# Optimization experiments

Hardware: AMD Instinct MI355X
Metric: run time of the kernel (lower is better)

The kernel has to match this reference:

```python
import jax, jax.numpy as jnp
import numpy as np

S = 1        # support_num
K = 20       # neighbor_num for conv stages
EPS_BN = 1e-5

def _normalize(x, axis):
    n = jnp.linalg.norm(x, axis=axis, keepdims=True)
    return x / jnp.maximum(n, 1e-12)

def _knn(verts, k):
    # verts: (b, v, 3) -> (b, v, k) nearest-neighbor indices excluding self
    sq = jnp.sum(verts * verts, axis=-1)                                   # (b, v)
    d = sq[:, :, None] + sq[:, None, :] - 2.0 * jnp.einsum('bic,bjc->bij', verts, verts)
    _, idx = jax.lax.top_k(-d, k + 1)                                      # smallest distances
    return idx[:, :, 1:]

def _gather(t, idx):
    # t: (b, v, c), idx: (b, v, n) -> (b, v, n, c)
    return jax.vmap(lambda tb, ib: tb[ib])(t, idx)

def _theta(nidx, verts, directions, out_c):
    # relu(cos angle) between normalized neighbor directions and support directions
    ndir = _normalize(_gather(verts, nidx) - verts[:, :, None, :], -1)     # (b, v, n, 3)
    sdir = _normalize(directions, 0)                                       # (3, S*out_c)
    th = jax.nn.relu(jnp.einsum('bvnc,ck->bvnk', ndir, sdir))
    b, v, n, _ = th.shape
    return th.reshape(b, v, n, S, out_c)

def _conv_surface(nidx, verts, directions, kernel_num):
    th = _theta(nidx, verts, directions, kernel_num)                       # (b,v,n,S,k)
    return th.max(axis=2).sum(axis=2)                                      # (b, v, k)

def _conv_layer(nidx, verts, fm, w, bias, directions, out_c):
    th = _theta(nidx, verts, directions, out_c)                            # (b,v,n,S,o)
    fout = fm @ w + bias                                                   # (b,v,(S+1)*o)
    center = fout[..., :out_c]
    support = _gather(fout[..., out_c:], nidx)                             # (b,v,n,S*o)
    b, v, n, _ = support.shape
    act = (th * support.reshape(b, v, n, S, out_c)).max(axis=2).sum(axis=2)
    return center + act

def _bn(x):
    # BatchNorm1d(affine=False) training-mode: per-channel over (batch, vertices)
    m = jnp.mean(x, axis=(0, 1))
    v = jnp.var(x, axis=(0, 1))
    return (x - m) * jax.lax.rsqrt(v + EPS_BN)

def _pool(verts, fm, rate, nk):
    nidx = _knn(verts, nk)
    pooled = _gather(fm, nidx).max(axis=2)
    pn = verts.shape[1] // rate
    # deterministic subsample (original uses randperm; fixed choice for a stable baseline)
    return verts[:, :pn], pooled[:, :pn]

def _forward(vertices, c0_dir, c1_w, c1_b, c1_dir, d1_w, c2_w, c2_b, c2_dir, d2_w,
             c3_w, c3_b, c3_dir, d3_w, c4_w, c4_b, c4_dir, d4_w,
             cls_w1, cls_b1, cls_g, cls_beta, cls_w2, cls_b2):
    verts = jnp.transpose(vertices, (0, 2, 1))                             # (b, N, 3)
    nidx = _knn(verts, K)
    fm0 = jax.nn.relu(_conv_surface(nidx, verts, c0_dir, 32))
    res1 = fm0 @ d1_w.T
    fm1 = jax.nn.relu(_bn(_conv_layer(nidx, verts, fm0, c1_w, c1_b, c1_dir, 64))) + res1
    verts, fm1 = _pool(verts, fm1, 4, 4)
    nidx = _knn(verts, K)
    res2 = fm1 @ d2_w.T
    fm2 = jax.nn.relu(_bn(_conv_layer(nidx, verts, fm1, c2_w, c2_b, c2_dir, 128))) + res2
    res3 = fm2 @ d3_w.T
    fm3 = jax.nn.relu(_bn(_conv_layer(nidx, verts, fm2, c3_w, c3_b, c3_dir, 256))) + res3
    verts, fm3 = _pool(verts, fm3, 4, 4)
    nidx = _knn(verts, K)
    res4 = fm3 @ d4_w.T
    fm4 = jax.nn.relu(_bn(_conv_layer(nidx, verts, fm3, c4_w, c4_b, c4_dir, 1024))) + res4
    g = fm4.max(axis=1)                                                    # (b, 1024)
    h = g @ cls_w1.T + cls_b1
    m = jnp.mean(h, axis=0); var = jnp.var(h, axis=0)                      # BN(256), dropout=eval identity
    h = (h - m) * jax.lax.rsqrt(var + EPS_BN) * cls_g + cls_beta
    h = jax.nn.relu(h)
    return h @ cls_w2.T + cls_b2                                           # (b, 40)

def setup_inputs() -> dict:
    key = jax.random.key(0)
    ks = jax.random.split(key, 24)
    def u(k, shape, s=0.05):
        return jax.random.uniform(k, shape, jnp.float32, -s, s)
    return {
        'vertices': jax.random.normal(ks[0], (32, 3, 1024), jnp.float32),
        'c0_dir': u(ks[1], (3, S * 32)),
        'c1_w': u(ks[2], (32, (S + 1) * 64)),  'c1_b': u(ks[3], ((S + 1) * 64,)),  'c1_dir': u(ks[4], (3, S * 64)),
        'd1_w': u(ks[5], (64, 32)),
        'c2_w': u(ks[6], (64, (S + 1) * 128)), 'c2_b': u(ks[7], ((S + 1) * 128,)), 'c2_dir': u(ks[8], (3, S * 128)),
        'd2_w': u(ks[9], (128, 64)),
        'c3_w': u(ks[10], (128, (S + 1) * 256)), 'c3_b': u(ks[11], ((S + 1) * 256,)), 'c3_dir': u(ks[12], (3, S * 256)),
        'd3_w': u(ks[13], (256, 128)),
        'c4_w': u(ks[14], (256, (S + 1) * 1024)), 'c4_b': u(ks[15], ((S + 1) * 1024,)), 'c4_dir': u(ks[16], (3, S * 1024)),
        'd4_w': u(ks[17], (1024, 256)),
        'cls_w1': u(ks[18], (256, 1024)), 'cls_b1': u(ks[19], (256,)),
        'cls_g': jnp.ones((256,), jnp.float32), 'cls_beta': jnp.zeros((256,), jnp.float32),
        'cls_w2': u(ks[20], (40, 256)), 'cls_b2': u(ks[21], (40,)),
    }

def reference(vertices, c0_dir, c1_w, c1_b, c1_dir, d1_w, c2_w, c2_b, c2_dir, d2_w,
              c3_w, c3_b, c3_dir, d3_w, c4_w, c4_b, c4_dir, d4_w,
              cls_w1, cls_b1, cls_g, cls_beta, cls_w2, cls_b2):
    return _forward(vertices, c0_dir, c1_w, c1_b, c1_dir, d1_w, c2_w, c2_b, c2_dir, d2_w,
                    c3_w, c3_b, c3_dir, d3_w, c4_w, c4_b, c4_dir, d4_w,
                    cls_w1, cls_b1, cls_g, cls_beta, cls_w2, cls_b2)
```

## Files before the change

kernel.cpp:

```cpp
#include <hip/hip_runtime.h>

#define TPB 256
#define KNN_TPB 512
static inline int nblk(long n) { return (int)((n + TPB - 1) / TPB); }

#define FINF 3.402823466e38f

template <int NS, bool WDIR, bool CSURF, int K2>
__device__ __forceinline__ void knn_body(int bx, int b, const float* __restrict__ vin,
                                         int* __restrict__ knn, float* __restrict__ ndir,
                                         int V_out, const float* __restrict__ c0dir,
                                         float* __restrict__ fm0, int V2, int* __restrict__ knn4,
                                         float4* pts, int (*sidx)[20], float (*sdir)[20][3],
                                         unsigned (*cdist)[256], unsigned short (*cidx)[256]) {
    constexpr int K = 20;
    constexpr int VF = NS * 64;
    const float* vb = vin + (size_t)b * 3072;
    for (int j = threadIdx.x; j < VF; j += blockDim.x) {
        float x = vb[j], y = vb[1024 + j], z = vb[2048 + j];
        pts[j] = make_float4(x, y, z, x * x + y * y + z * z);
    }
    __syncthreads();
    int lane = threadIdx.x & 63;
    int w = threadIdx.x >> 6;
    int i = bx * 8 + w;
    if (i >= V_out) return;
    float4 pi = pts[i];
    unsigned ud[NS];
    unsigned lmin = 0xFFFFFFFFu;
#pragma unroll
    for (int s = 0; s < NS; ++s) {
        int j = s * 64 + lane;
        float4 pj = pts[j];
        float dist = pi.w + pj.w - 2.f * (pi.x * pj.x + pi.y * pj.y + pi.z * pj.z);
        dist = fmaxf(dist, 0.f);
        unsigned v = (j == i) ? 0xFFFFFFFFu : __float_as_uint(dist);
        ud[s] = v;
        lmin = v < lmin ? v : lmin;
    }
    unsigned pmin = lmin;
    {
        unsigned o = (unsigned)__shfl_xor((int)pmin, 1, 64);
        pmin = o < pmin ? o : pmin;
    }
    unsigned gmin = lmin, M = pmin;
#pragma unroll
    for (int off = 32; off > 1; off >>= 1) {
        unsigned on = (unsigned)__shfl_xor((int)gmin, off, 64);
        gmin = on < gmin ? on : gmin;
        unsigned om = (unsigned)__shfl_xor((int)M, off, 64);
        M = om > M ? om : M;
    }
    {
        unsigned on = (unsigned)__shfl_xor((int)gmin, 1, 64);
        gmin = on < gmin ? on : gmin;
    }
    int* orow = knn + ((size_t)(b * V_out + i)) * K;
    unsigned long long lmask = (1ull << lane) - 1ull;
    bool done = false;
    if constexpr (NS >= 8) {
        int cnt = 0;
#pragma unroll
        for (int s = 0; s < NS; ++s) {
            unsigned long long mm = __ballot(ud[s] <= M);
            if (ud[s] <= M) {
                int p = cnt + __popcll(mm & lmask);
                if (p < 256) { cdist[w][p] = ud[s]; cidx[w][p] = (unsigned short)(s * 64 + lane); }
            }
            cnt += __popcll(mm);
        }
        if (cnt <= 256) {
            unsigned cd[4];
#pragma unroll
            for (int r = 0; r < 4; ++r) {
                int p = lane + r * 64;
                cd[r] = p < cnt ? cdist[w][p] : 0xFFFFFFFFu;
            }
            unsigned lo = gmin, hi = M + 1u;
            while (hi - lo > 1u) {
                unsigned mid = lo + ((hi - lo) >> 1);
                int c = 0;
#pragma unroll
                for (int r = 0; r < 4; ++r)
                    c += __popcll(__ballot(cd[r] < mid));
                if (c >= K) hi = mid; else lo = mid;
            }
            unsigned T = lo;
            int base = 0;
#pragma unroll
            for (int r = 0; r < 4; ++r) {
                unsigned long long mm = __ballot(cd[r] < T);
                if (cd[r] < T) {
                    int p = base + __popcll(mm & lmask);
                    int j = cidx[w][lane + r * 64];
                    sidx[w][p] = j; orow[p] = j;
                }
                base += __popcll(mm);
            }
            int need = K - base, run = 0;
#pragma unroll
            for (int r = 0; r < 4; ++r) {
                unsigned long long mm = __ballot(cd[r] == T);
                int rr = run + __popcll(mm & lmask);
                if (cd[r] == T && rr < need) {
                    int j = cidx[w][lane + r * 64];
                    sidx[w][base + rr] = j; orow[base + rr] = j;
                }
                run += __popcll(mm);
            }
            done = true;
        }
    }
    if (!done) {
        unsigned lo = gmin, hi = M + 1u;
        while (hi - lo > 1u) {
            unsigned mid = lo + ((hi - lo) >> 1);
            int cnt = 0;
#pragma unroll
            for (int s = 0; s < NS; ++s)
                cnt += __popcll(__ballot(ud[s] < mid));
            if (cnt >= K) hi = mid; else lo = mid;
        }
        unsigned T = lo;
        int base = 0;
#pragma unroll
        for (int s = 0; s < NS; ++s) {
            unsigned long long m = __ballot(ud[s] < T);
            if (ud[s] < T) {
                int p = base + __popcll(m & lmask);
                sidx[w][p] = s * 64 + lane;
                orow[p] = s * 64 + lane;
            }
            base += __popcll(m);
        }
        int need = K - base, run = 0;
#pragma unroll
        for (int s = 0; s < NS; ++s) {
            unsigned long long m = __ballot(ud[s] == T);
            int r = run + __popcll(m & lmask);
            if (ud[s] == T && r < need) {
                sidx[w][base + r] = s * 64 + lane;
                orow[base + r] = s * 64 + lane;
            }
            run += __popcll(m);
        }
    }
    if (WDIR) {
        if (lane < K) {
            int j = sidx[w][lane];
            float4 pj = pts[j];
            float dx = pj.x - pi.x, dy = pj.y - pi.y, dz = pj.z - pi.z;
            float inv = 1.f / fmaxf(sqrtf(dx * dx + dy * dy + dz * dz), 1e-12f);
            float* o = ndir + ((size_t)(b * V_out + i) * K + lane) * 3;
            float nx = dx * inv, ny = dy * inv, nz = dz * inv;
            o[0] = nx; o[1] = ny; o[2] = nz;
            if (CSURF) { sdir[w][lane][0] = nx; sdir[w][lane][1] = ny; sdir[w][lane][2] = nz; }
        }
        if (CSURF && lane < 32) {
            int c = lane;
            float d0 = c0dir[c], d1 = c0dir[32 + c], d2 = c0dir[64 + c];
            float inv = 1.f / fmaxf(sqrtf(d0 * d0 + d1 * d1 + d2 * d2), 1e-12f);
            d0 *= inv; d1 *= inv; d2 *= inv;
            float m = 0.f;
            for (int n = 0; n < K; ++n) {
                float th = sdir[w][n][0] * d0 + sdir[w][n][1] * d1 + sdir[w][n][2] * d2;
                m = fmaxf(m, th);
            }
            fm0[(size_t)(b * V_out + i) * 32 + c] = m;
        }
    }
    if (K2 > 0 && i < V2) {
        float dsel = FINF;
        int jsel = 0x7FFFFFFF;
        if (lane < K) {
            jsel = sidx[w][lane];
            float4 pj = pts[jsel];
            dsel = fmaxf(pi.w + pj.w - 2.f * (pi.x * pj.x + pi.y * pj.y + pi.z * pj.z), 0.f);
        }
        int rank = 0;
        for (int m = 0; m < K; ++m) {
            float dm = __shfl(dsel, m, 64);
            int jm = __shfl(jsel, m, 64);
            rank += (dm < dsel || (dm == dsel && jm < jsel)) ? 1 : 0;
        }
        if (lane < K && rank < K2) knn4[((size_t)(b * V2 + i)) * K2 + rank] = jsel;
    }
}

__global__ __launch_bounds__(KNN_TPB, 1) void prep_kernel(const float* __restrict__ vin, const float* __restrict__ c0dir,
                                                          int* __restrict__ knn1, float* __restrict__ ndir1,
                                                          float* __restrict__ fm0, int* __restrict__ knn4_1,
                                                          int* __restrict__ knn2, float* __restrict__ ndir2,
                                                          int* __restrict__ knn4_2,
                                                          int* __restrict__ knn3, float* __restrict__ ndir3,
                                                          const float* __restrict__ d1, const float* __restrict__ d2,
                                                          const float* __restrict__ d3, const float* __restrict__ d4,
                                                          float* __restrict__ o1, float* __restrict__ o2,
                                                          float* __restrict__ o3, float* __restrict__ o4,
                                                          float* __restrict__ pz) {
    __shared__ float4 pts[1024];
    __shared__ int sidx[8][20];
    __shared__ float sdir[8][20][3];
    __shared__ unsigned cdist[8][256];
    __shared__ unsigned short cidx[8][256];
    int bx = blockIdx.x, b = blockIdx.y;
    if (bx < 128) {
        knn_body<16, true, true, 4>(bx, b, vin, knn1, ndir1, 1024, c0dir, fm0, 256, knn4_1,
                                    pts, sidx, sdir, cdist, cidx);
        return;
    }
    if (bx < 160) {
        knn_body<4, true, false, 4>(bx - 128, b, vin, knn2, ndir2, 256, nullptr, nullptr, 64, knn4_2,
                                    pts, sidx, sdir, cdist, cidx);
        return;
    }
    if (bx < 168) {
        knn_body<1, true, false, 0>(bx - 160, b, vin, knn3, ndir3, 64, nullptr, nullptr, 0, nullptr,
                                    pts, sidx, sdir, cdist, cidx);
        return;
    }
    if (b != 0) return;
    if (bx < 764) {
        int t = (bx - 168) * KNN_TPB + threadIdx.x;
        if (t < 2048) { int r = t / 32, c = t % 32; o1[c * 64 + r] = d1[t]; return; }
        int t2 = t - 2048;
        if (t2 < 8192) { int r = t2 / 64, c = t2 % 64; o2[c * 128 + r] = d2[t2]; return; }
        int t3 = t2 - 8192;
        if (t3 < 32768) { int r = t3 / 128, c = t3 % 128; o3[c * 256 + r] = d3[t3]; return; }
        int t4 = t3 - 32768;
        if (t4 < 262144) { int r = t4 / 256, c = t4 % 256; o4[c * 1024 + r] = d4[t4]; }
        return;
    }
    int t5 = (bx - 764) * KNN_TPB + threadIdx.x;
    if (t5 < 57344) pz[t5] = 0.f;
}

template <int MODE>
__global__ __launch_bounds__(TPB) void gemm64_kernel(const float* __restrict__ A, const float* __restrict__ W,
                                                     const float* __restrict__ bias,
                                                     const float* __restrict__ conv, const float* __restrict__ partial,
                                                     float* __restrict__ out, int M, int N, int K, int nsplit) {
    __shared__ float As[64][36];
    __shared__ float Bs[32][68];
    __shared__ float smean[64], sinv[64];
    int t = threadIdx.x;
    int tx = t & 15, ty = t >> 4;
    int colbase = blockIdx.x * 64, rowbase = blockIdx.y * 64;
    int r0 = ty * 4, c0 = tx * 4;
    if constexpr (MODE >= 1) {
        __shared__ double sred[2][4][64];
        int cc = t & 63, g = t >> 6;
        double s = 0.0, ss = 0.0;
        for (int sp = g; sp < nsplit; sp += 4) {
            s += partial[(size_t)sp * 2 * N + colbase + cc];
            ss += partial[(size_t)sp * 2 * N + N + colbase + cc];
        }
        sred[0][g][cc] = s; sred[1][g][cc] = ss;
        __syncthreads();
        if (t < 64) {
            double S = sred[0][0][t] + sred[0][1][t] + sred[0][2][t] + sred[0][3][t];
            double SS = sred[1][0][t] + sred[1][1][t] + sred[1][2][t] + sred[1][3][t];
            double mean = S / M;
            double var = SS / M - mean * mean;
            if (var < 0) var = 0;
            smean[t] = (float)mean;
            sinv[t] = rsqrtf((float)var + 1e-5f);
        }
        __syncthreads();
    }
    float4 acc0, acc1, acc2, acc3;
    if (MODE == 0) {
        float4 bv = *(const float4*)(bias + colbase + c0);
        acc0 = bv; acc1 = bv; acc2 = bv; acc3 = bv;
    } else {
        acc0 = make_float4(0.f, 0.f, 0.f, 0.f); acc1 = acc0; acc2 = acc0; acc3 = acc0;
    }
    for (int kt = 0; kt < K; kt += 32) {
#pragma unroll
        for (int l = 0; l < 2; ++l) {
            int lin = t + l * 256;
            int ar = lin >> 3, ak = (lin & 7) << 2;
            *(float4*)&As[ar][ak] = *(const float4*)(A + (size_t)(rowbase + ar) * K + kt + ak);
            int br = lin >> 4, bn = (lin & 15) << 2;
            *(float4*)&Bs[br][bn] = *(const float4*)(W + (size_t)(kt + br) * N + colbase + bn);
        }
        __syncthreads();
#pragma unroll 4
        for (int k = 0; k < 32; ++k) {
            float4 bv = *(const float4*)&Bs[k][c0];
            float a0 = As[r0][k], a1 = As[r0 + 1][k], a2 = As[r0 + 2][k], a3 = As[r0 + 3][k];
            acc0.x += a0 * bv.x; acc0.y += a0 * bv.y; acc0.z += a0 * bv.z; acc0.w += a0 * bv.w;
            acc1.x += a1 * bv.x; acc1.y += a1 * bv.y; acc1.z += a1 * bv.z; acc1.w += a1 * bv.w;
            acc2.x += a2 * bv.x; acc2.y += a2 * bv.y; acc2.z += a2 * bv.z; acc2.w += a2 * bv.w;
            acc3.x += a3 * bv.x; acc3.y += a3 * bv.y; acc3.z += a3 * bv.z; acc3.w += a3 * bv.w;
        }
        __syncthreads();
    }
    float4 accs[4] = {acc0, acc1, acc2, acc3};
    if constexpr (MODE >= 1) {
        float4 mean = *(const float4*)&smean[c0];
        float4 inv = *(const float4*)&sinv[c0];
#pragma unroll
        for (int rr = 0; rr < 4; ++rr) {
            float4 cv = *(const float4*)(conv + (size_t)(rowbase + r0 + rr) * N + colbase + c0);
            accs[rr].x += fmaxf((cv.x - mean.x) * inv.x, 0.f);
            accs[rr].y += fmaxf((cv.y - mean.y) * inv.y, 0.f);
            accs[rr].z += fmaxf((cv.z - mean.z) * inv.z, 0.f);
            accs[rr].w += fmaxf((cv.w - mean.w) * inv.w, 0.f);
        }
    }
    if constexpr (MODE == 2) {
        __shared__ float redmax[16][68];
        float4 tm;
        tm.x = fmaxf(fmaxf(accs[0].x, accs[1].x), fmaxf(accs[2].x, accs[3].x));
        tm.y = fmaxf(fmaxf(accs[0].y, accs[1].y), fmaxf(accs[2].y, accs[3].y));
        tm.z = fmaxf(fmaxf(accs[0].z, accs[1].z), fmaxf(accs[2].z, accs[3].z));
        tm.w = fmaxf(fmaxf(accs[0].w, accs[1].w), fmaxf(accs[2].w, accs[3].w));
        *(float4*)&redmax[ty][c0] = tm;
        __syncthreads();
        if (t < 64) {
            float m = redmax[0][t];
#pragma unroll
            for (int g = 1; g < 16; ++g) m = fmaxf(m, redmax[g][t]);
            out[(size_t)blockIdx.y * N + colbase + t] = m;
        }
    } else {
#pragma unroll
        for (int rr = 0; rr < 4; ++rr)
            *(float4*)(out + (size_t)(rowbase + r0 + rr) * N + colbase + c0) = accs[rr];
    }
}

template <bool FUSE>
__global__ __launch_bounds__(TPB) void conv_act_kernel(const float* __restrict__ ndir, const int* __restrict__ knn,
                                const float* __restrict__ fout, const float* __restrict__ dir,
                                float* __restrict__ out, int B, int Vst, int K, int Cout,
                                float* __restrict__ bnpart) {
    __shared__ float sAcc[2][256];
    int t = blockIdx.x * blockDim.x + threadIdx.x;
    int nc4 = Cout >> 2;
    bool active = t < B * Vst * nc4;
    float4 o = make_float4(0.f, 0.f, 0.f, 0.f);
    int c4 = 0;
    if (active) {
        int row = t / nc4; c4 = (t % nc4) * 4;
        int b = row / Vst;
        float4 D0 = *(const float4*)(dir + c4);
        float4 D1 = *(const float4*)(dir + Cout + c4);
        float4 D2 = *(const float4*)(dir + 2 * Cout + c4);
        float4 e0, e1, e2;
        {
            float i0 = 1.f / fmaxf(sqrtf(D0.x * D0.x + D1.x * D1.x + D2.x * D2.x), 1e-12f);
            float i1 = 1.f / fmaxf(sqrtf(D0.y * D0.y + D1.y * D1.y + D2.y * D2.y), 1e-12f);
            float i2 = 1.f / fmaxf(sqrtf(D0.z * D0.z + D1.z * D1.z + D2.z * D2.z), 1e-12f);
            float i3 = 1.f / fmaxf(sqrtf(D0.w * D0.w + D1.w * D1.w + D2.w * D2.w), 1e-12f);
            e0 = make_float4(D0.x * i0, D0.y * i1, D0.z * i2, D0.w * i3);
            e1 = make_float4(D1.x * i0, D1.y * i1, D1.z * i2, D1.w * i3);
            e2 = make_float4(D2.x * i0, D2.y * i1, D2.z * i2, D2.w * i3);
        }
        int Cw = 2 * Cout;
        float4 m = make_float4(-FINF, -FINF, -FINF, -FINF);
        const float* nd = ndir + (size_t)row * K * 3;
        const int* kr = knn + (size_t)row * K;
        for (int n = 0; n < K; ++n) {
            int j = kr[n];
            float n0 = nd[n * 3], n1 = nd[n * 3 + 1], n2 = nd[n * 3 + 2];
            float4 s = *(const float4*)(fout + ((size_t)(b * Vst + j)) * Cw + Cout + c4);
            float t0 = fmaxf(n0 * e0.x + n1 * e1.x + n2 * e2.x, 0.f);
            float t1 = fmaxf(n0 * e0.y + n1 * e1.y + n2 * e2.y, 0.f);
            float t2 = fmaxf(n0 * e0.z + n1 * e1.z + n2 * e2.z, 0.f);
            float t3 = fmaxf(n0 * e0.w + n1 * e1.w + n2 * e2.w, 0.f);
            m.x = fmaxf(m.x, t0 * s.x);
            m.y = fmaxf(m.y, t1 * s.y);
            m.z = fmaxf(m.z, t2 * s.z);
            m.w = fmaxf(m.w, t3 * s.w);
        }
        float4 ctr = *(const float4*)(fout + (size_t)row * Cw + c4);
        o = make_float4(ctr.x + m.x, ctr.y + m.y, ctr.z + m.z, ctr.w + m.w);
        *(float4*)(out + (size_t)row * Cout + c4) = o;
    }
    if constexpr (FUSE) {
        for (int i = threadIdx.x; i < 2 * Cout; i += TPB) ((float*)sAcc)[i < Cout ? i : 256 + (i - Cout)] = 0.f;
        __syncthreads();
        if (active) {
            atomicAdd(&sAcc[0][c4 + 0], o.x); atomicAdd(&sAcc[1][c4 + 0], o.x * o.x);
            atomicAdd(&sAcc[0][c4 + 1], o.y); atomicAdd(&sAcc[1][c4 + 1], o.y * o.y);
            atomicAdd(&sAcc[0][c4 + 2], o.z); atomicAdd(&sAcc[1][c4 + 2], o.z * o.z);
            atomicAdd(&sAcc[0][c4 + 3], o.w); atomicAdd(&sAcc[1][c4 + 3], o.w * o.w);
        }
        __syncthreads();
        int bin = blockIdx.x & 63;
        for (int i = threadIdx.x; i < Cout; i += TPB) {
            atomicAdd(&bnpart[(size_t)bin * 2 * Cout + i], sAcc[0][i]);
            atomicAdd(&bnpart[(size_t)bin * 2 * Cout + Cout + i], sAcc[1][i]);
        }
    }
}

__global__ __launch_bounds__(TPB) void bn_partial_kernel(const float* __restrict__ x, float* __restrict__ partial,
                                                         int rows, int C, int nsplit) {
    int t = blockIdx.x * blockDim.x + threadIdx.x;
    if (t >= C * nsplit) return;
    int c = t % C, sp = t / C;
    int chunk = rows / nsplit;
    int r0 = sp * chunk;
    float s = 0.f, ss = 0.f;
    for (int r = r0; r < r0 + chunk; ++r) {
        float v = x[(size_t)r * C + c];
        s += v; ss += v * v;
    }
    partial[(size_t)sp * 2 * C + c] = s;
    partial[(size_t)sp * 2 * C + C + c] = ss;
}

__global__ __launch_bounds__(TPB) void pool_max_kernel(const float* __restrict__ fm, const int* __restrict__ knn4,
                                float* __restrict__ out, int B, int Vin, int pn, int C) {
    int t = blockIdx.x * blockDim.x + threadIdx.x;
    if (t >= B * pn * C) return;
    int row = t / C, c = t % C;
    int b = row / pn;
    const int* kr = knn4 + (size_t)row * 4;
    float m = fmaxf(fmaxf(fm[((size_t)(b * Vin + kr[0])) * C + c], fm[((size_t)(b * Vin + kr[1])) * C + c]),
                    fmaxf(fm[((size_t)(b * Vin + kr[2])) * C + c], fm[((size_t)(b * Vin + kr[3])) * C + c]));
    out[t] = m;
}

__global__ __launch_bounds__(TPB, 1) void gemm_t_wave_kernel(const float* __restrict__ in, const float* __restrict__ w,
                                   const float* __restrict__ bias, float* __restrict__ out,
                                   int rows, int Cin, int Cout) {
    int wid = (blockIdx.x * blockDim.x + threadIdx.x) >> 6;
    int lane = threadIdx.x & 63;
    if (wid >= rows * Cout) return;
    int r = wid / Cout, c = wid % Cout;
    const float4* a = (const float4*)(in + (size_t)r * Cin);
    const float4* wr = (const float4*)(w + (size_t)c * Cin);
    int n4 = Cin >> 2;
    float acc = 0.f;
    for (int k = lane; k < n4; k += 64) {
        float4 av = a[k], wv = wr[k];
        acc += av.x * wv.x + av.y * wv.y + av.z * wv.z + av.w * wv.w;
    }
#pragma unroll
    for (int off = 32; off > 0; off >>= 1) acc += __shfl_xor(acc, off, 64);
    if (lane == 0) out[wid] = acc + bias[c];
}

__global__ __launch_bounds__(TPB, 1) void cls_fused_kernel(const float* __restrict__ h,
                                 const float* __restrict__ gam, const float* __restrict__ beta,
                                 const float* __restrict__ w2, const float* __restrict__ b2,
                                 float* __restrict__ out) {
    __shared__ float smean[256], sa[256];
    int t = threadIdx.x;
    {
        float s = 0.f, ss = 0.f;
        for (int b = 0; b < 32; ++b) {
            float v = h[(size_t)b * 256 + t];
            s += v; ss += v * v;
        }
        float mn = s / 32.f;
        float var = ss / 32.f - mn * mn;
        if (var < 0.f) var = 0.f;
        smean[t] = mn;
        sa[t] = rsqrtf(var + 1e-5f) * gam[t];
    }
    __syncthreads();
    int wid = blockIdx.x * 4 + (t >> 6);
    int lane = t & 63;
    if (wid >= 32 * 40) return;
    int b = wid / 40, o = wid % 40;
    float acc = 0.f;
#pragma unroll
    for (int kk = 0; kk < 4; ++kk) {
        int c = lane + kk * 64;
        float v = fmaxf((h[b * 256 + c] - smean[c]) * sa[c] + beta[c], 0.f);
        acc += v * w2[o * 256 + c];
    }
#pragma unroll
    for (int off = 32; off > 0; off >>= 1) acc += __shfl_xor(acc, off, 64);
    if (lane == 0) out[wid] = acc + b2[o];
}

extern "C" void kernel_launch(void* const* d_in, const int* in_sizes, int n_in,
                              void* d_out, int out_size, void* d_ws, size_t ws_size,
                              hipStream_t stream) {
    const float* vertices = (const float*)d_in[0];
    const float* c0_dir = (const float*)d_in[1];
    const float* c1_w  = (const float*)d_in[2];
    const float* c1_b  = (const float*)d_in[3];
    const float* c1_dir = (const float*)d_in[4];
    const float* d1_w  = (const float*)d_in[5];
    const float* c2_w  = (const float*)d_in[6];
    const float* c2_b  = (const float*)d_in[7];
    const float* c2_dir = (const float*)d_in[8];
    const float* d2_w  = (const float*)d_in[9];
    const float* c3_w  = (const float*)d_in[10];
    const float* c3_b  = (const float*)d_in[11];
    const float* c3_dir = (const float*)d_in[12];
    const float* d3_w  = (const float*)d_in[13];
    const float* c4_w  = (const float*)d_in[14];
    const float* c4_b  = (const float*)d_in[15];
    const float* c4_dir = (const float*)d_in[16];
    const float* d4_w  = (const float*)d_in[17];
    const float* cls_w1 = (const float*)d_in[18];
    const float* cls_b1 = (const float*)d_in[19];
    const float* cls_g  = (const float*)d_in[20];
    const float* cls_beta = (const float*)d_in[21];
    const float* cls_w2 = (const float*)d_in[22];
    const float* cls_b2 = (const float*)d_in[23];

    const int B = 32;
    float* ws = (float*)d_ws;
    size_t off = 0;
    auto alloc = [&](size_t n) { float* p = ws + off; off += n; return p; };
    int*   knn1  = (int*)alloc(655360);
    int*   knn2  = (int*)alloc(163840);
    int*   knn3  = (int*)alloc(40960);
    int*   knn4_1 = (int*)alloc(32768);
    int*   knn4_2 = (int*)alloc(8192);
    float* ndir1 = alloc(1966080);
    float* ndir2 = alloc(491520);
    float* ndir3 = alloc(122880);
    float* fm0   = alloc(1048576);
    float* fm1   = alloc(2097152);
    float* fm1p  = alloc(524288);
    float* fm2   = alloc(1048576);
    float* fm3   = alloc(2097152);
    float* fm3p  = alloc(524288);
    float* fout  = alloc(4194304);
    float* convp = alloc(2097152);
    float* gbuf  = alloc(32768);
    float* hbuf  = alloc(8192);
    float* d1t   = alloc(2048);
    float* d2t   = alloc(8192);
    float* d3t   = alloc(32768);
    float* d4t   = alloc(262144);
    float* pz    = alloc(57344);
    float* p1    = pz;
    float* p2a   = pz + 8192;
    float* p2b   = pz + 24576;
    float* partial3 = alloc(131072);

    prep_kernel<<<dim3(876, B), KNN_TPB, 0, stream>>>(
        vertices, c0_dir, knn1, ndir1, fm0, knn4_1, knn2, ndir2, knn4_2, knn3, ndir3,
        d1_w, d2_w, d3_w, d4_w, d1t, d2t, d3t, d4t, pz);

    gemm64_kernel<0><<<dim3(2, 512), TPB, 0, stream>>>(fm0, c1_w, c1_b, nullptr, nullptr, fout, B * 1024, 128, 32, 0);
    conv_act_kernel<true><<<nblk((long)B * 1024 * 16), TPB, 0, stream>>>(ndir1, knn1, fout, c1_dir, convp, B, 1024, 20, 64, p1);
    gemm64_kernel<1><<<dim3(1, 512), TPB, 0, stream>>>(fm0, d1t, nullptr, convp, p1, fm1, B * 1024, 64, 32, 64);
    pool_max_kernel<<<nblk((long)B * 256 * 64), TPB, 0, stream>>>(fm1, knn4_1, fm1p, B, 1024, 256, 64);

    gemm64_kernel<0><<<dim3(4, 128), TPB, 0, stream>>>(fm1p, c2_w, c2_b, nullptr, nullptr, fout, B * 256, 256, 64, 0);
    conv_act_kernel<true><<<nblk((long)B * 256 * 32), TPB, 0, stream>>>(ndir2, knn2, fout, c2_dir, convp, B, 256, 20, 128, p2a);
    gemm64_kernel<1><<<dim3(2, 128), TPB, 0, stream>>>(fm1p, d2t, nullptr, convp, p2a, fm2, B * 256, 128, 64, 64);
    gemm64_kernel<0><<<dim3(8, 128), TPB, 0, stream>>>(fm2, c3_w, c3_b, nullptr, nullptr, fout, B * 256, 512, 128, 0);
    conv_act_kernel<true><<<nblk((long)B * 256 * 64), TPB, 0, stream>>>(ndir2, knn2, fout, c3_dir, convp, B, 256, 20, 256, p2b);
    gemm64_kernel<1><<<dim3(4, 128), TPB, 0, stream>>>(fm2, d3t, nullptr, convp, p2b, fm3, B * 256, 256, 128, 64);
    pool_max_kernel<<<nblk((long)B * 64 * 256), TPB, 0, stream>>>(fm3, knn4_2, fm3p, B, 256, 64, 256);

    gemm64_kernel<0><<<dim3(32, 32), TPB, 0, stream>>>(fm3p, c4_w, c4_b, nullptr, nullptr, fout, B * 64, 2048, 256, 0);
    conv_act_kernel<false><<<nblk((long)B * 64 * 256), TPB, 0, stream>>>(ndir3, knn3, fout, c4_dir, convp, B, 64, 20, 1024, nullptr);
    bn_partial_kernel<<<nblk(1024 * 64), TPB, 0, stream>>>(convp, partial3, B * 64, 1024, 64);
    gemm64_kernel<2><<<dim3(16, 32), TPB, 0, stream>>>(fm3p, d4t, nullptr, convp, partial3, gbuf, B * 64, 1024, 256, 64);

    gemm_t_wave_kernel<<<nblk((long)32 * 256 * 64), TPB, 0, stream>>>(gbuf, cls_w1, cls_b1, hbuf, 32, 1024, 256);
    cls_fused_kernel<<<320, TPB, 0, stream>>>(hbuf, cls_g, cls_beta, cls_w2, cls_b2, (float*)d_out);
}
```

Before: 344.3 us.

## Fuse stage-4 BN statistics into conv activation kernel and skip empty KNN rounds

```diff
diff --git a/kernel.cpp b/kernel.cpp
--- a/kernel.cpp
+++ b/kernel.cpp
@@ -82,31 +82,36 @@
                 int c = 0;
 #pragma unroll
                 for (int r = 0; r < 4; ++r)
-                    c += __popcll(__ballot(cd[r] < mid));
+                    if (r * 64 < cnt)
+                        c += __popcll(__ballot(cd[r] < mid));
                 if (c >= K) hi = mid; else lo = mid;
             }
             unsigned T = lo;
             int base = 0;
 #pragma unroll
             for (int r = 0; r < 4; ++r) {
-                unsigned long long mm = __ballot(cd[r] < T);
-                if (cd[r] < T) {
-                    int p = base + __popcll(mm & lmask);
-                    int j = cidx[w][lane + r * 64];
-                    sidx[w][p] = j; orow[p] = j;
+                if (r * 64 < cnt) {
+                    unsigned long long mm = __ballot(cd[r] < T);
+                    if (cd[r] < T) {
+                        int p = base + __popcll(mm & lmask);
+                        int j = cidx[w][lane + r * 64];
+                        sidx[w][p] = j; orow[p] = j;
+                    }
+                    base += __popcll(mm);
                 }
-                base += __popcll(mm);
             }
             int need = K - base, run = 0;
 #pragma unroll
             for (int r = 0; r < 4; ++r) {
-                unsigned long long mm = __ballot(cd[r] == T);
-                int rr = run + __popcll(mm & lmask);
-                if (cd[r] == T && rr < need) {
-                    int j = cidx[w][lane + r * 64];
-                    sidx[w][base + rr] = j; orow[base + rr] = j;
+                if (r * 64 < cnt) {
+                    unsigned long long mm = __ballot(cd[r] == T);
+                    int rr = run + __popcll(mm & lmask);
+                    if (cd[r] == T && rr < need) {
+                        int j = cidx[w][lane + r * 64];
+                        sidx[w][base + rr] = j; orow[base + rr] = j;
+                    }
+                    run += __popcll(mm);
                 }
-                run += __popcll(mm);
             }
             done = true;
         }
@@ -232,7 +237,7 @@
         return;
     }
     int t5 = (bx - 764) * KNN_TPB + threadIdx.x;
-    if (t5 < 57344) pz[t5] = 0.f;
+    if (t5 < 188416) pz[t5] = 0.f;
 }
 
 template <int MODE>
@@ -397,20 +402,61 @@
     }
 }
 
-__global__ __launch_bounds__(TPB) void bn_partial_kernel(const float* __restrict__ x, float* __restrict__ partial,
-                                                         int rows, int C, int nsplit) {
-    int t = blockIdx.x * blockDim.x + threadIdx.x;
-    if (t >= C * nsplit) return;
-    int c = t % C, sp = t / C;
-    int chunk = rows / nsplit;
-    int r0 = sp * chunk;
-    float s = 0.f, ss = 0.f;
-    for (int r = r0; r < r0 + chunk; ++r) {
-        float v = x[(size_t)r * C + c];
-        s += v; ss += v * v;
-    }
-    partial[(size_t)sp * 2 * C + c] = s;
-    partial[(size_t)sp * 2 * C + C + c] = ss;
+__global__ __launch_bounds__(TPB) void conv_act_s3_kernel(const float* __restrict__ ndir, const int* __restrict__ knn,
+                                                          const float* __restrict__ fout, const float* __restrict__ dir,
+                                                          float* __restrict__ out, float* __restrict__ bnpart) {
+    constexpr int Cout = 1024, K = 20, Vst = 64, Cw = 2048;
+    __shared__ float sAcc[2][256];
+    sAcc[0][threadIdx.x] = 0.f;
+    sAcc[1][threadIdx.x] = 0.f;
+    __syncthreads();
+    int bid = blockIdx.x;
+    int rg = bid >> 2, cslice = bid & 3;
+    int row = rg * 4 + (threadIdx.x >> 6);
+    int lc4 = threadIdx.x & 63;
+    int c4 = cslice * 256 + lc4 * 4;
+    int b = row / Vst;
+    float4 D0 = *(const float4*)(dir + c4);
+    float4 D1 = *(const float4*)(dir + Cout + c4);
+    float4 D2 = *(const float4*)(dir + 2 * Cout + c4);
+    float4 e0, e1, e2;
+    {
+        float i0 = 1.f / fmaxf(sqrtf(D0.x * D0.x + D1.x * D1.x + D2.x * D2.x), 1e-12f);
+        float i1 = 1.f / fmaxf(sqrtf(D0.y * D0.y + D1.y * D1.y + D2.y * D2.y), 1e-12f);
+        float i2 = 1.f / fmaxf(sqrtf(D0.z * D0.z + D1.z * D1.z + D2.z * D2.z), 1e-12f);
+        float i3 = 1.f / fmaxf(sqrtf(D0.w * D0.w + D1.w * D1.w + D2.w * D2.w), 1e-12f);
+        e0 = make_float4(D0.x * i0, D0.y * i1, D0.z * i2, D0.w * i3);
+        e1 = make_float4(D1.x * i0, D1.y * i1, D1.z * i2, D1.w * i3);
+        e2 = make_float4(D2.x * i0, D2.y * i1, D2.z * i2, D2.w * i3);
+    }
+    float4 m = make_float4(-FINF, -FINF, -FINF, -FINF);
+    const float* nd = ndir + (size_t)row * K * 3;
+    const int* kr = knn + (size_t)row * K;
+    for (int n = 0; n < K; ++n) {
+        int j = kr[n];
+        float n0 = nd[n * 3], n1 = nd[n * 3 + 1], n2 = nd[n * 3 + 2];
+        float4 s = *(const float4*)(fout + ((size_t)(b * Vst + j)) * Cw + Cout + c4);
+        float t0 = fmaxf(n0 * e0.x + n1 * e1.x + n2 * e2.x, 0.f);
+        float t1 = fmaxf(n0 * e0.y + n1 * e1.y + n2 * e2.y, 0.f);
+        float t2 = fmaxf(n0 * e0.z + n1 * e1.z + n2 * e2.z, 0.f);
+        float t3 = fmaxf(n0 * e0.w + n1 * e1.w + n2 * e2.w, 0.f);
+        m.x = fmaxf(m.x, t0 * s.x);
+        m.y = fmaxf(m.y, t1 * s.y);
+        m.z = fmaxf(m.z, t2 * s.z);
+        m.w = fmaxf(m.w, t3 * s.w);
+    }
+    float4 ctr = *(const float4*)(fout + (size_t)row * Cw + c4);
+    float4 o = make_float4(ctr.x + m.x, ctr.y + m.y, ctr.z + m.z, ctr.w + m.w);
+    *(float4*)(out + (size_t)row * Cout + c4) = o;
+    int lc = lc4 * 4;
+    atomicAdd(&sAcc[0][lc + 0], o.x); atomicAdd(&sAcc[1][lc + 0], o.x * o.x);
+    atomicAdd(&sAcc[0][lc + 1], o.y); atomicAdd(&sAcc[1][lc + 1], o.y * o.y);
+    atomicAdd(&sAcc[0][lc + 2], o.z); atomicAdd(&sAcc[1][lc + 2], o.z * o.z);
+    atomicAdd(&sAcc[0][lc + 3], o.w); atomicAdd(&sAcc[1][lc + 3], o.w * o.w);
+    __syncthreads();
+    int bin = bid & 63;
+    atomicAdd(&bnpart[(size_t)bin * 2048 + cslice * 256 + threadIdx.x], sAcc[0][threadIdx.x]);
+    atomicAdd(&bnpart[(size_t)bin * 2048 + 1024 + cslice * 256 + threadIdx.x], sAcc[1][threadIdx.x]);
 }
 
 __global__ __launch_bounds__(TPB) void pool_max_kernel(const float* __restrict__ fm, const int* __restrict__ knn4,
@@ -534,13 +580,13 @@
     float* d2t   = alloc(8192);
     float* d3t   = alloc(32768);
     float* d4t   = alloc(262144);
-    float* pz    = alloc(57344);
+    float* pz    = alloc(188416);
     float* p1    = pz;
     float* p2a   = pz + 8192;
     float* p2b   = pz + 24576;
-    float* partial3 = alloc(131072);
-
-    prep_kernel<<<dim3(876, B), KNN_TPB, 0, stream>>>(
+    float* p3    = pz + 57344;
+
+    prep_kernel<<<dim3(1132, B), KNN_TPB, 0, stream>>>(
         vertices, c0_dir, knn1, ndir1, fm0, knn4_1, knn2, ndir2, knn4_2, knn3, ndir3,
         d1_w, d2_w, d3_w, d4_w, d1t, d2t, d3t, d4t, pz);
 
@@ -558,9 +604,8 @@
     pool_max_kernel<<<nblk((long)B * 64 * 256), TPB, 0, stream>>>(fm3, knn4_2, fm3p, B, 256, 64, 256);
 
     gemm64_kernel<0><<<dim3(32, 32), TPB, 0, stream>>>(fm3p, c4_w, c4_b, nullptr, nullptr, fout, B * 64, 2048, 256, 0);
-    conv_act_kernel<false><<<nblk((long)B * 64 * 256), TPB, 0, stream>>>(ndir3, knn3, fout, c4_dir, convp, B, 64, 20, 1024, nullptr);
-    bn_partial_kernel<<<nblk(1024 * 64), TPB, 0, stream>>>(convp, partial3, B * 64, 1024, 64);
-    gemm64_kernel<2><<<dim3(16, 32), TPB, 0, stream>>>(fm3p, d4t, nullptr, convp, partial3, gbuf, B * 64, 1024, 256, 64);
+    conv_act_s3_kernel<<<2048, TPB, 0, stream>>>(ndir3, knn3, fout, c4_dir, convp, p3);
+    gemm64_kernel<2><<<dim3(16, 32), TPB, 0, stream>>>(fm3p, d4t, nullptr, convp, p3, gbuf, B * 64, 1024, 256, 64);
 
     gemm_t_wave_kernel<<<nblk((long)32 * 256 * 64), TPB, 0, stream>>>(gbuf, cls_w1, cls_b1, hbuf, 32, 1024, 256);
     cls_fused_kernel<<<320, TPB, 0, stream>>>(hbuf, cls_g, cls_beta, cls_w2, cls_b2, (float*)d_out);
```

Measured after the change: 356.4 us. +3.5%, slower.
